# Kernel tuning notes

Measured on AMD Instinct MI355X. Metric: run time of the kernel, lower is better.

Reference implementation:

```python
import jax, jax.numpy as jnp
import numpy as np
import math

# ---- GPT-OSS attention config (gpt-oss-20b) ----
HIDDEN = 2880
HEAD_DIM = 64
N_Q_HEADS = 64
N_KV_HEADS = 8
GROUP = N_Q_HEADS // N_KV_HEADS  # 8
WINDOW = 128                      # sliding window (keys in (q-128, q])
ROPE_BASE = 150000.0
SCALING_FACTOR = 32.0
NTK_ALPHA = 1.0
NTK_BETA = 32.0
INIT_CTX = 4096
Q_SIZE = N_Q_HEADS * HEAD_DIM     # 4096
KV_SIZE = N_KV_HEADS * HEAD_DIM   # 512
SM_SCALE = HEAD_DIM ** -0.5


def _yarn_inv_freq_and_concentration():
    """YaRN-scaled inverse frequencies (matches GptOssRotaryEmbedding)."""
    d_half = HEAD_DIM / 2
    freq = ROPE_BASE ** (np.arange(0, HEAD_DIM, 2, dtype=np.float32) / HEAD_DIM)
    concentration = 0.1 * math.log(SCALING_FACTOR) + 1.0
    low = d_half * math.log(INIT_CTX / (NTK_BETA * 2 * math.pi)) / math.log(ROPE_BASE)
    high = d_half * math.log(INIT_CTX / (NTK_ALPHA * 2 * math.pi)) / math.log(ROPE_BASE)
    interpolation = 1.0 / (SCALING_FACTOR * freq)
    extrapolation = 1.0 / freq
    ramp = (np.arange(d_half, dtype=np.float32) - low) / (high - low)
    mask = 1.0 - np.clip(ramp, 0.0, 1.0)
    inv_freq = interpolation * (1.0 - mask) + extrapolation * mask
    return jnp.asarray(inv_freq, jnp.float32), jnp.float32(concentration)

_INV_FREQ, _CONC = _yarn_inv_freq_and_concentration()


def _apply_rope(x, cos, sin):
    # x: [n, h, d]; cos/sin: [n, d/2] (neox style: rotate halves)
    d2 = HEAD_DIM // 2
    x1, x2 = x[..., :d2], x[..., d2:]
    c, s = cos[:, None, :], sin[:, None, :]
    return jnp.concatenate([x1 * c - x2 * s, x2 * c + x1 * s], axis=-1)


def setup_inputs() -> dict:
    key = jax.random.key(0)
    ks = jax.random.split(key, 6)
    n = 8192
    return {
        "hidden_states": jax.random.normal(ks[0], (n, HIDDEN), jnp.float32),
        "position_ids": jnp.arange(n, dtype=jnp.int32),
        "qkv_w": jax.random.normal(ks[1], (Q_SIZE + 2 * KV_SIZE, HIDDEN), jnp.float32) * (HIDDEN ** -0.5),
        "qkv_b": jax.random.normal(ks[2], (Q_SIZE + 2 * KV_SIZE,), jnp.float32) * 0.02,
        "o_w": jax.random.normal(ks[3], (HIDDEN, Q_SIZE), jnp.float32) * (Q_SIZE ** -0.5),
        "o_b": jax.random.normal(ks[4], (HIDDEN,), jnp.float32) * 0.02,
        "sinks": jax.random.normal(ks[5], (N_Q_HEADS,), jnp.float32),
    }


def reference(hidden_states, position_ids, qkv_w, qkv_b, o_w, o_b, sinks):
    n = hidden_states.shape[0]
    W = WINDOW
    nb = n // W  # n must be a multiple of the window (8192 / 128 = 64)

    # QKV projection
    qkv = hidden_states @ qkv_w.T + qkv_b
    q = qkv[:, :Q_SIZE].reshape(n, N_Q_HEADS, HEAD_DIM)
    k = qkv[:, Q_SIZE:Q_SIZE + KV_SIZE].reshape(n, N_KV_HEADS, HEAD_DIM)
    v = qkv[:, Q_SIZE + KV_SIZE:].reshape(n, N_KV_HEADS, HEAD_DIM)

    # RoPE (YaRN, neox)
    angles = position_ids.astype(jnp.float32)[:, None] * _INV_FREQ[None, :]
    cos = jnp.cos(angles) * _CONC
    sin = jnp.sin(angles) * _CONC
    q = _apply_rope(q, cos, sin)
    k = _apply_rope(k, cos, sin)

    # Blocked sliding-window attention: each W-block of queries attends to
    # [previous block, own block] keys (window=W keys incl. self).
    qb = (q * SM_SCALE).reshape(nb, W, N_KV_HEADS, GROUP, HEAD_DIM)
    kb = k.reshape(nb, W, N_KV_HEADS, HEAD_DIM)
    vb = v.reshape(nb, W, N_KV_HEADS, HEAD_DIM)
    k2 = jnp.concatenate([jnp.concatenate([jnp.zeros_like(kb[:1]), kb[:-1]], 0), kb], axis=1)  # [nb,2W,Hk,d]
    v2 = jnp.concatenate([jnp.concatenate([jnp.zeros_like(vb[:1]), vb[:-1]], 0), vb], axis=1)

    # scores: [nb, Hk, G, W, 2W]
    scores = jnp.einsum('bqgjd,bkgd->bgjqk', qb, k2)

    # mask: key global idx = (b-1)*W + j; need 0 <= q-k <= W-1 and k >= 0
    i = jnp.arange(W)[:, None]
    j = jnp.arange(2 * W)[None, :]
    mrel = (j >= i + 1) & (j <= i + W)                       # [W, 2W]
    first = (jnp.arange(nb)[:, None, None] > 0) | (j >= W)   # [nb, 1|W, 2W]
    mask = (mrel[None] & first)[:, None, None, :, :]          # [nb,1,1,W,2W]

    neg_inf = jnp.float32(-jnp.inf)
    s = jnp.where(mask, scores, neg_inf)
    sink = sinks.reshape(N_KV_HEADS, GROUP)[None, :, :, None]  # [1,Hk,G,1]
    m = jnp.maximum(jnp.max(s, axis=-1), sink)                  # [nb,Hk,G,W]
    e = jnp.exp(s - m[..., None])
    denom = e.sum(axis=-1) + jnp.exp(sink - m)                  # sink adds to denominator only
    p = e / denom[..., None]

    out = jnp.einsum('bgjqk,bkgd->bqgjd', p, v2).reshape(n, Q_SIZE)
    return out @ o_w.T + o_b
```

## Files before the change

### kernel.cpp

```cpp
#include <hip/hip_runtime.h>
#include <math.h>
#include <stdint.h>

typedef float  f32x4  __attribute__((ext_vector_type(4)));
typedef __bf16 bf16x8 __attribute__((ext_vector_type(8)));
typedef __bf16 bf16x4 __attribute__((ext_vector_type(4)));

#define MFMA16(a, b, c) __builtin_amdgcn_mfma_f32_16x16x32_bf16(a, b, c, 0, 0, 0)

__device__ __forceinline__ void async16(const void* g, void* l) {
  __builtin_amdgcn_global_load_lds((__attribute__((address_space(1))) void*)g,
                                   (__attribute__((address_space(3))) void*)l,
                                   16, 0, 0);
}

__global__ __launch_bounds__(256) void cast_f32_to_bf16(const float* __restrict__ in,
                                                        __bf16* __restrict__ out, int n) {
  int idx = (blockIdx.x * 256 + threadIdx.x) * 4;
  if (idx + 3 < n) {
    float4 v = *(const float4*)(in + idx);
    bf16x4 o;
    o[0] = (__bf16)v.x; o[1] = (__bf16)v.y; o[2] = (__bf16)v.z; o[3] = (__bf16)v.w;
    *(bf16x4*)(out + idx) = o;
  }
}

__global__ __launch_bounds__(256) void rope_table_kernel(const int* __restrict__ pos_ids,
                                                         float2* __restrict__ tab, int total) {
  int idx = blockIdx.x * 256 + threadIdx.x;
  if (idx >= total) return;
  int p = idx >> 5, d = idx & 31;
  float posf = (float)pos_ids[p];
  float ex = (float)(2 * d) * (1.0f / 64.0f);
  float freq = powf(150000.0f, ex);
  float inv_scaled = 1.0f / (32.0f * freq);
  float inv_plain = 1.0f / freq;
  float lr = logf(150000.0f);
  const float TWO_PI = 6.28318530717958647692f;
  float low  = 32.0f * logf(4096.0f / (32.0f * TWO_PI)) / lr;
  float high = 32.0f * logf(4096.0f / TWO_PI) / lr;
  float ramp = ((float)d - low) / (high - low);
  ramp = fminf(fmaxf(ramp, 0.0f), 1.0f);
  float maskv = 1.0f - ramp;
  float inv_freq = inv_scaled * (1.0f - maskv) + inv_plain * maskv;
  float conc = 0.1f * logf(32.0f) + 1.0f;
  float ang = posf * inv_freq;
  float s, c;
  sincosf(ang, &s, &c);
  tab[idx] = make_float2(c * conc, s * conc);
}

template <typename OutT, bool DO_ROPE>
__global__ __launch_bounds__(512, 2) void gemm256(const __bf16* __restrict__ A,
                                                  const __bf16* __restrict__ B,
                                                  const float* __restrict__ bias,
                                                  OutT* __restrict__ C,
                                                  const float2* __restrict__ tab,
                                                  int M, int N, int K) {
  __shared__ __align__(16) __bf16 lds_all[65536];
  __bf16* Asl = lds_all;
  __bf16* Bsl = lds_all + 32768;

  const int tid = threadIdx.x;
  const int wv  = tid >> 6;
  const int ln  = tid & 63;
  const int l16 = ln & 15;
  const int quad = ln >> 4;
  const int wr = wv >> 2;
  const int wc = wv & 3;

  const int nTN = (N + 255) >> 8;
  int bid = (int)blockIdx.x;
  int nwg = (int)gridDim.x;
  int swz = bid;
  if ((nwg & 7) == 0) {
    int cpx = nwg >> 3;
    swz = (bid & 7) * cpx + (bid >> 3);
  }
  const int brow = swz / nTN;
  const int bcol = swz % nTN;
  const int row0 = brow << 8, col0 = bcol << 8;

  const int rsw  = (l16 >> 1) & 3;
  const int aoff = (wr * 128 + l16) * 32 + ((quad ^ rsw) * 8);
  const int boff = (wc * 64 + l16) * 32 + ((quad ^ rsw) * 8);

  const int srow = tid >> 2;
  const int skq  = (tid & 3) ^ ((tid >> 3) & 3);

  auto stA = [&](int t_, int kh) {
    const __bf16* s = A + (size_t)(row0 + srow) * K + t_ * 64 + kh * 32 + skq * 8;
    char* d = (char*)Asl + (((2 * t_ + kh) & 3) << 14) + (wv << 10);
    async16(s, d);
    async16(s + (size_t)128 * K, d + 8192);
  };
  auto stB = [&](int t_, int kh) {
    int r0 = col0 + srow;       if (r0 > N - 1) r0 = N - 1;
    int r1 = col0 + srow + 128; if (r1 > N - 1) r1 = N - 1;
    const int kb = t_ * 64 + kh * 32 + skq * 8;
    char* d = (char*)Bsl + (((2 * t_ + kh) & 3) << 14) + (wv << 10);
    async16(B + (size_t)r0 * K + kb, d);
    async16(B + (size_t)r1 * K + kb, d + 8192);
  };

  f32x4 acc[8][4];
#pragma unroll
  for (int t = 0; t < 8; t++)
#pragma unroll
    for (int u = 0; u < 4; u++) acc[t][u] = (f32x4){0.f, 0.f, 0.f, 0.f};

  const int nt = K >> 6;

  stA(0, 0); stB(0, 0); stA(0, 1); stB(0, 1);
  if (nt > 1) {
    stA(1, 0); stB(1, 0); stA(1, 1); stB(1, 1);
    asm volatile("s_waitcnt vmcnt(4)" ::: "memory");
  } else {
    asm volatile("s_waitcnt vmcnt(0)" ::: "memory");
  }
  __builtin_amdgcn_s_barrier();

#define PHASE_TAIL()                                      \
  __builtin_amdgcn_s_barrier();                           \
  asm volatile("s_waitcnt lgkmcnt(0)" ::: "memory");      \
  __builtin_amdgcn_sched_barrier(0);                      \
  __builtin_amdgcn_s_setprio(1);

#define PHASE_END()                                       \
  __builtin_amdgcn_s_setprio(0);                          \
  __builtin_amdgcn_s_barrier();

#pragma unroll 1
  for (int t = 0; t < nt; ++t) {
    const __bf16* As0 = Asl + (((2 * t) & 3) << 13);
    const __bf16* Bs0 = Bsl + (((2 * t) & 3) << 13);
    const __bf16* As1 = Asl + (((2 * t + 1) & 3) << 13);
    const __bf16* Bs1 = Bsl + (((2 * t + 1) & 3) << 13);
    bf16x8 a[8], b0, b1;

#pragma unroll
    for (int tt = 0; tt < 8; ++tt) a[tt] = *(const bf16x8*)(As0 + aoff + tt * 512);
    b0 = *(const bf16x8*)(Bs0 + boff);
    b1 = *(const bf16x8*)(Bs0 + boff + 512);
    if (t >= 1 && t + 1 < nt) stA(t + 1, 1);
    PHASE_TAIL();
#pragma unroll
    for (int tt = 0; tt < 8; ++tt) {
      acc[tt][0] = MFMA16(a[tt], b0, acc[tt][0]);
      acc[tt][1] = MFMA16(a[tt], b1, acc[tt][1]);
    }
    PHASE_END();

    b0 = *(const bf16x8*)(Bs0 + boff + 1024);
    b1 = *(const bf16x8*)(Bs0 + boff + 1536);
    if (t >= 1 && t + 1 < nt) stB(t + 1, 1);
    PHASE_TAIL();
#pragma unroll
    for (int tt = 0; tt < 8; ++tt) {
      acc[tt][2] = MFMA16(a[tt], b0, acc[tt][2]);
      acc[tt][3] = MFMA16(a[tt], b1, acc[tt][3]);
    }
    PHASE_END();

#pragma unroll
    for (int tt = 0; tt < 8; ++tt) a[tt] = *(const bf16x8*)(As1 + aoff + tt * 512);
    b0 = *(const bf16x8*)(Bs1 + boff);
    b1 = *(const bf16x8*)(Bs1 + boff + 512);
    if (t + 2 < nt) stA(t + 2, 0);
    PHASE_TAIL();
#pragma unroll
    for (int tt = 0; tt < 8; ++tt) {
      acc[tt][0] = MFMA16(a[tt], b0, acc[tt][0]);
      acc[tt][1] = MFMA16(a[tt], b1, acc[tt][1]);
    }
    PHASE_END();

    b0 = *(const bf16x8*)(Bs1 + boff + 1024);
    b1 = *(const bf16x8*)(Bs1 + boff + 1536);
    if (t + 2 < nt) {
      stB(t + 2, 0);
      asm volatile("s_waitcnt vmcnt(4)" ::: "memory");
    } else {
      asm volatile("s_waitcnt vmcnt(0)" ::: "memory");
    }
    PHASE_TAIL();
#pragma unroll
    for (int tt = 0; tt < 8; ++tt) {
      acc[tt][2] = MFMA16(a[tt], b0, acc[tt][2]);
      acc[tt][3] = MFMA16(a[tt], b1, acc[tt][3]);
    }
    PHASE_END();
  }
#undef PHASE_TAIL
#undef PHASE_END

  const int hh = (col0 + wc * 64) >> 6;
  if (DO_ROPE && hh < 72) {
    const float scale = hh < 64 ? 0.125f : 1.0f;
    float bv[4];
#pragma unroll
    for (int u = 0; u < 4; u++) bv[u] = bias[col0 + wc * 64 + u * 16 + l16];
#pragma unroll
    for (int tt = 0; tt < 8; ++tt) {
      int rowb = row0 + wr * 128 + tt * 16 + quad * 4;
#pragma unroll
      for (int r = 0; r < 4; r++) {
        int row = rowb + r;
#pragma unroll
        for (int u = 0; u < 2; u++) {
          float2 cs = tab[row * 32 + u * 16 + l16];
          float x1 = acc[tt][u][r] + bv[u];
          float x2 = acc[tt][u + 2][r] + bv[u + 2];
          C[(size_t)row * N + col0 + wc * 64 + u * 16 + l16] =
              (OutT)((x1 * cs.x - x2 * cs.y) * scale);
          C[(size_t)row * N + col0 + wc * 64 + (u + 2) * 16 + l16] =
              (OutT)((x2 * cs.x + x1 * cs.y) * scale);
        }
      }
    }
  } else {
#pragma unroll
    for (int u = 0; u < 4; u++) {
      int col = col0 + wc * 64 + u * 16 + l16;
      if (col < N) {
        float bv = bias[col];
#pragma unroll
        for (int tt = 0; tt < 8; ++tt) {
          int row = row0 + wr * 128 + tt * 16 + quad * 4;
#pragma unroll
          for (int r = 0; r < 4; r++)
            C[(size_t)(row + r) * N + col] = (OutT)(acc[tt][u][r] + bv);
        }
      }
    }
  }
}

__global__ __launch_bounds__(256) void attn_kernel(const __bf16* __restrict__ qkv,
                                                   const float* __restrict__ sinks,
                                                   __bf16* __restrict__ out) {
  __shared__ __align__(16) __bf16 vT_s[64 * 264];
  __shared__ __align__(16) __bf16 p_s[64 * 136];
  const int tid = threadIdx.x;
  const int bh = blockIdx.x >> 1;
  const int qh = blockIdx.x & 1;
  const int b = bh >> 3;
  const int h = bh & 7;
  const int wv = tid >> 6;
  const int ln = tid & 63;
  const int l16 = ln & 15;
  const int quad = ln >> 4;

  for (int c = tid; c < 2048; c += 256) {
    int key = c >> 3, dc = c & 7;
    int vpos = b * 128 + key - 128;
    bf16x8 vv = {};
    if (vpos >= 0)
      vv = *(const bf16x8*)(qkv + (size_t)vpos * 5120 + 4608 + h * 64 + dc * 8);
    int keysw = key ^ ((dc & 3) << 3);
#pragma unroll
    for (int l2 = 0; l2 < 8; l2++)
      vT_s[(dc * 8 + l2) * 264 + keysw] = vv[l2];
  }
  __syncthreads();

#pragma unroll 1
  for (int pass = 0; pass < 8; pass++) {
    int g = qh * 4 + (pass >> 1);
    int i0 = (pass & 1) * 64 + wv * 16;
    int head = h * 8 + g;
    float sink = sinks[head];

    size_t qbase = (size_t)(b * 128 + i0 + l16) * 5120 + head * 64;
    bf16x8 aq0 = *(const bf16x8*)(qkv + qbase + quad * 8);
    bf16x8 aq1 = *(const bf16x8*)(qkv + qbase + 32 + quad * 8);

    f32x4 sc[16];
#pragma unroll
    for (int ct = 0; ct < 16; ct++) {
      int key = ct * 16 + l16;
      int kpos = b * 128 + key - 128;
      if (kpos < 0) kpos = 0;
      const __bf16* kp = qkv + (size_t)kpos * 5120 + 4096 + h * 64;
      bf16x8 kb0 = *(const bf16x8*)(kp + quad * 8);
      bf16x8 kb1 = *(const bf16x8*)(kp + 32 + quad * 8);
      f32x4 z = (f32x4){0.f, 0.f, 0.f, 0.f};
      __builtin_amdgcn_s_setprio(1);
      z = MFMA16(aq0, kb0, z);
      z = MFMA16(aq1, kb1, z);
      __builtin_amdgcn_s_setprio(0);
      sc[ct] = z;
    }

    float mx[4] = {-INFINITY, -INFINITY, -INFINITY, -INFINITY};
#pragma unroll
    for (int ct = 0; ct < 16; ct++) {
      int j = ct * 16 + l16;
#pragma unroll
      for (int r = 0; r < 4; r++) {
        int i = i0 + quad * 4 + r;
        bool valid = (j >= i + 1) && (j <= i + 128) && (b > 0 || j >= 128);
        float s = valid ? sc[ct][r] : -INFINITY;
        sc[ct][r] = s;
        mx[r] = fmaxf(mx[r], s);
      }
    }
#pragma unroll
    for (int off = 1; off < 16; off <<= 1)
#pragma unroll
      for (int r = 0; r < 4; r++)
        mx[r] = fmaxf(mx[r], __shfl_xor(mx[r], off));
#pragma unroll
    for (int r = 0; r < 4; r++) mx[r] = fmaxf(mx[r], sink);

    float sum[4] = {0.f, 0.f, 0.f, 0.f};
#pragma unroll
    for (int ct = 0; ct < 16; ct++)
#pragma unroll
      for (int r = 0; r < 4; r++) {
        float e = __expf(sc[ct][r] - mx[r]);
        sc[ct][r] = e;
        sum[r] += e;
      }
#pragma unroll
    for (int off = 1; off < 16; off <<= 1)
#pragma unroll
      for (int r = 0; r < 4; r++)
        sum[r] += __shfl_xor(sum[r], off);

    f32x4 o[4];
#pragma unroll
    for (int dt = 0; dt < 4; dt++) o[dt] = (f32x4){0.f, 0.f, 0.f, 0.f};
#pragma unroll 1
    for (int kh = 0; kh < 2; kh++) {
#pragma unroll
      for (int ct = 0; ct < 8; ct++)
#pragma unroll
        for (int r = 0; r < 4; r++)
          p_s[(wv * 16 + quad * 4 + r) * 136 + ct * 16 + l16] = (__bf16)sc[kh * 8 + ct][r];
#pragma unroll
      for (int ks = 0; ks < 4; ks++) {
        bf16x8 pa = *(const bf16x8*)&p_s[(wv * 16 + l16) * 136 + ks * 32 + quad * 8];
        __builtin_amdgcn_s_setprio(1);
#pragma unroll
        for (int dt = 0; dt < 4; dt++) {
          int sw = ((dt * 2 + (l16 >> 3)) & 3) << 3;
          bf16x8 vb = *(const bf16x8*)&vT_s[(dt * 16 + l16) * 264 +
                                            ((kh * 128 + ks * 32 + quad * 8) ^ sw)];
          o[dt] = MFMA16(pa, vb, o[dt]);
        }
        __builtin_amdgcn_s_setprio(0);
      }
    }

#pragma unroll
    for (int r = 0; r < 4; r++) {
      float rd = 1.0f / (sum[r] + __expf(sink - mx[r]));
      int posn = b * 128 + i0 + quad * 4 + r;
      size_t obase = (size_t)posn * 4096 + head * 64;
#pragma unroll
      for (int dt = 0; dt < 4; dt++)
        out[obase + dt * 16 + l16] = (__bf16)(o[dt][r] * rd);
    }
  }
}

extern "C" void kernel_launch(void* const* d_in, const int* in_sizes, int n_in,
                              void* d_out, int out_size, void* d_ws, size_t ws_size,
                              hipStream_t stream) {
  (void)in_sizes; (void)n_in; (void)out_size; (void)ws_size;
  const float* hs     = (const float*)d_in[0];
  const int*   pos    = (const int*)d_in[1];
  const float* qkv_w  = (const float*)d_in[2];
  const float* qkv_b  = (const float*)d_in[3];
  const float* o_w    = (const float*)d_in[4];
  const float* o_b    = (const float*)d_in[5];
  const float* sinks  = (const float*)d_in[6];
  float* outp = (float*)d_out;
  char* ws = (char*)d_ws;

  const size_t O_QKV = 0;
  const size_t O_ATT = 83886080;
  const size_t O_TAB = 131072000;
  const size_t O_W   = 150994944;
  __bf16* qkvb = (__bf16*)(ws + O_QKV);
  __bf16* hsb  = (__bf16*)(ws + O_ATT);
  __bf16* attn = (__bf16*)(ws + O_ATT);
  float2* tab  = (float2*)(ws + O_TAB);
  __bf16* wb   = (__bf16*)(ws + O_W);

  cast_f32_to_bf16<<<23040, 256, 0, stream>>>(hs, hsb, 8192 * 2880);
  cast_f32_to_bf16<<<14400, 256, 0, stream>>>(qkv_w, wb, 5120 * 2880);
  rope_table_kernel<<<1024, 256, 0, stream>>>(pos, tab, 8192 * 32);
  gemm256<__bf16, true><<<640, 512, 0, stream>>>(hsb, wb, qkv_b, qkvb, tab,
                                                 8192, 5120, 2880);
  cast_f32_to_bf16<<<11520, 256, 0, stream>>>(o_w, wb, 2880 * 4096);
  attn_kernel<<<1024, 256, 0, stream>>>(qkvb, sinks, attn);
  gemm256<float, false><<<384, 512, 0, stream>>>(attn, wb, o_b, outp, nullptr,
                                                 8192, 2880, 4096);
}
```

Baseline: 926.4 us.

## Stage K in swizzled LDS for attention and reorder GEMM MFMA phases

The attention kernel now loads the K window into a swizzled shared-memory tile once per block, alongside V, instead of reading K from global memory in every pass. This removes repeated global loads of the same keys across the eight passes. The P staging buffer is shrunk by processing keys in four chunks of 64 rather than two of 128. The GEMM main loop is reorganised into 4x4 MFMA quadrants that reload A fragments instead of B fragments, and the sched_barrier is dropped so the compiler can interleave LDS reads with MFMAs, at the cost of more LDS use and different register pressure.

```diff
diff --git a/kernel.cpp b/kernel.cpp
--- a/kernel.cpp
+++ b/kernel.cpp
@@ -123,7 +123,6 @@
 #define PHASE_TAIL()                                      \
   __builtin_amdgcn_s_barrier();                           \
   asm volatile("s_waitcnt lgkmcnt(0)" ::: "memory");      \
-  __builtin_amdgcn_sched_barrier(0);                      \
   __builtin_amdgcn_s_setprio(1);
 
 #define PHASE_END()                                       \
@@ -136,47 +135,44 @@
     const __bf16* Bs0 = Bsl + (((2 * t) & 3) << 13);
     const __bf16* As1 = Asl + (((2 * t + 1) & 3) << 13);
     const __bf16* Bs1 = Bsl + (((2 * t + 1) & 3) << 13);
-    bf16x8 a[8], b0, b1;
-
-#pragma unroll
-    for (int tt = 0; tt < 8; ++tt) a[tt] = *(const bf16x8*)(As0 + aoff + tt * 512);
-    b0 = *(const bf16x8*)(Bs0 + boff);
-    b1 = *(const bf16x8*)(Bs0 + boff + 512);
+    bf16x8 a[4], b[4];
+
+#pragma unroll
+    for (int i = 0; i < 4; ++i) a[i] = *(const bf16x8*)(As0 + aoff + i * 512);
+#pragma unroll
+    for (int u = 0; u < 4; ++u) b[u] = *(const bf16x8*)(Bs0 + boff + u * 512);
     if (t >= 1 && t + 1 < nt) stA(t + 1, 1);
     PHASE_TAIL();
 #pragma unroll
-    for (int tt = 0; tt < 8; ++tt) {
-      acc[tt][0] = MFMA16(a[tt], b0, acc[tt][0]);
-      acc[tt][1] = MFMA16(a[tt], b1, acc[tt][1]);
-    }
+    for (int i = 0; i < 4; ++i)
+#pragma unroll
+      for (int u = 0; u < 4; ++u) acc[i][u] = MFMA16(a[i], b[u], acc[i][u]);
     PHASE_END();
 
-    b0 = *(const bf16x8*)(Bs0 + boff + 1024);
-    b1 = *(const bf16x8*)(Bs0 + boff + 1536);
+#pragma unroll
+    for (int i = 0; i < 4; ++i) a[i] = *(const bf16x8*)(As0 + aoff + (4 + i) * 512);
     if (t >= 1 && t + 1 < nt) stB(t + 1, 1);
     PHASE_TAIL();
 #pragma unroll
-    for (int tt = 0; tt < 8; ++tt) {
-      acc[tt][2] = MFMA16(a[tt], b0, acc[tt][2]);
-      acc[tt][3] = MFMA16(a[tt], b1, acc[tt][3]);
-    }
+    for (int i = 0; i < 4; ++i)
+#pragma unroll
+      for (int u = 0; u < 4; ++u) acc[4 + i][u] = MFMA16(a[i], b[u], acc[4 + i][u]);
     PHASE_END();
 
 #pragma unroll
-    for (int tt = 0; tt < 8; ++tt) a[tt] = *(const bf16x8*)(As1 + aoff + tt * 512);
-    b0 = *(const bf16x8*)(Bs1 + boff);
-    b1 = *(const bf16x8*)(Bs1 + boff + 512);
+    for (int i = 0; i < 4; ++i) a[i] = *(const bf16x8*)(As1 + aoff + i * 512);
+#pragma unroll
+    for (int u = 0; u < 4; ++u) b[u] = *(const bf16x8*)(Bs1 + boff + u * 512);
     if (t + 2 < nt) stA(t + 2, 0);
     PHASE_TAIL();
 #pragma unroll
-    for (int tt = 0; tt < 8; ++tt) {
-      acc[tt][0] = MFMA16(a[tt], b0, acc[tt][0]);
-      acc[tt][1] = MFMA16(a[tt], b1, acc[tt][1]);
-    }
+    for (int i = 0; i < 4; ++i)
+#pragma unroll
+      for (int u = 0; u < 4; ++u) acc[i][u] = MFMA16(a[i], b[u], acc[i][u]);
     PHASE_END();
 
-    b0 = *(const bf16x8*)(Bs1 + boff + 1024);
-    b1 = *(const bf16x8*)(Bs1 + boff + 1536);
+#pragma unroll
+    for (int i = 0; i < 4; ++i) a[i] = *(const bf16x8*)(As1 + aoff + (4 + i) * 512);
     if (t + 2 < nt) {
       stB(t + 2, 0);
       asm volatile("s_waitcnt vmcnt(4)" ::: "memory");
@@ -185,10 +181,9 @@
     }
     PHASE_TAIL();
 #pragma unroll
-    for (int tt = 0; tt < 8; ++tt) {
-      acc[tt][2] = MFMA16(a[tt], b0, acc[tt][2]);
-      acc[tt][3] = MFMA16(a[tt], b1, acc[tt][3]);
-    }
+    for (int i = 0; i < 4; ++i)
+#pragma unroll
+      for (int u = 0; u < 4; ++u) acc[4 + i][u] = MFMA16(a[i], b[u], acc[4 + i][u]);
     PHASE_END();
   }
 #undef PHASE_TAIL
@@ -240,7 +235,8 @@
                                                    const float* __restrict__ sinks,
                                                    __bf16* __restrict__ out) {
   __shared__ __align__(16) __bf16 vT_s[64 * 264];
-  __shared__ __align__(16) __bf16 p_s[64 * 136];
+  __shared__ __align__(16) __bf16 k_s[256 * 64];
+  __shared__ __align__(16) __bf16 p_s[64 * 72];
   const int tid = threadIdx.x;
   const int bh = blockIdx.x >> 1;
   const int qh = blockIdx.x & 1;
@@ -253,14 +249,18 @@
 
   for (int c = tid; c < 2048; c += 256) {
     int key = c >> 3, dc = c & 7;
-    int vpos = b * 128 + key - 128;
-    bf16x8 vv = {};
-    if (vpos >= 0)
-      vv = *(const bf16x8*)(qkv + (size_t)vpos * 5120 + 4608 + h * 64 + dc * 8);
+    int pos = b * 128 + key - 128;
+    bf16x8 vv = {}, kk = {};
+    if (pos >= 0) {
+      const __bf16* base = qkv + (size_t)pos * 5120 + h * 64 + dc * 8;
+      kk = *(const bf16x8*)(base + 4096);
+      vv = *(const bf16x8*)(base + 4608);
+    }
     int keysw = key ^ ((dc & 3) << 3);
 #pragma unroll
     for (int l2 = 0; l2 < 8; l2++)
       vT_s[(dc * 8 + l2) * 264 + keysw] = vv[l2];
+    *(bf16x8*)&k_s[key * 64 + ((dc ^ (key & 7)) * 8)] = kk;
   }
   __syncthreads();
 
@@ -276,14 +276,12 @@
     bf16x8 aq1 = *(const bf16x8*)(qkv + qbase + 32 + quad * 8);
 
     f32x4 sc[16];
+    const int sw0 = (quad ^ (l16 & 7)) * 8;
 #pragma unroll
     for (int ct = 0; ct < 16; ct++) {
-      int key = ct * 16 + l16;
-      int kpos = b * 128 + key - 128;
-      if (kpos < 0) kpos = 0;
-      const __bf16* kp = qkv + (size_t)kpos * 5120 + 4096 + h * 64;
-      bf16x8 kb0 = *(const bf16x8*)(kp + quad * 8);
-      bf16x8 kb1 = *(const bf16x8*)(kp + 32 + quad * 8);
+      const __bf16* kp = &k_s[(ct * 16 + l16) * 64];
+      bf16x8 kb0 = *(const bf16x8*)(kp + sw0);
+      bf16x8 kb1 = *(const bf16x8*)(kp + (sw0 ^ 32));
       f32x4 z = (f32x4){0.f, 0.f, 0.f, 0.f};
       __builtin_amdgcn_s_setprio(1);
       z = MFMA16(aq0, kb0, z);
@@ -331,22 +329,22 @@
     f32x4 o[4];
 #pragma unroll
     for (int dt = 0; dt < 4; dt++) o[dt] = (f32x4){0.f, 0.f, 0.f, 0.f};
-#pragma unroll 1
-    for (int kh = 0; kh < 2; kh++) {
-#pragma unroll
-      for (int ct = 0; ct < 8; ct++)
+#pragma unroll
+    for (int q = 0; q < 4; q++) {
+#pragma unroll
+      for (int ct = 0; ct < 4; ct++)
 #pragma unroll
         for (int r = 0; r < 4; r++)
-          p_s[(wv * 16 + quad * 4 + r) * 136 + ct * 16 + l16] = (__bf16)sc[kh * 8 + ct][r];
-#pragma unroll
-      for (int ks = 0; ks < 4; ks++) {
-        bf16x8 pa = *(const bf16x8*)&p_s[(wv * 16 + l16) * 136 + ks * 32 + quad * 8];
+          p_s[(wv * 16 + quad * 4 + r) * 72 + ct * 16 + l16] = (__bf16)sc[q * 4 + ct][r];
+#pragma unroll
+      for (int ks = 0; ks < 2; ks++) {
+        bf16x8 pa = *(const bf16x8*)&p_s[(wv * 16 + l16) * 72 + ks * 32 + quad * 8];
         __builtin_amdgcn_s_setprio(1);
 #pragma unroll
         for (int dt = 0; dt < 4; dt++) {
+          int kk = q * 64 + ks * 32 + quad * 8;
           int sw = ((dt * 2 + (l16 >> 3)) & 3) << 3;
-          bf16x8 vb = *(const bf16x8*)&vT_s[(dt * 16 + l16) * 264 +
-                                            ((kh * 128 + ks * 32 + quad * 8) ^ sw)];
+          bf16x8 vb = *(const bf16x8*)&vT_s[(dt * 16 + l16) * 264 + (kk ^ sw)];
           o[dt] = MFMA16(pa, vb, o[dt]);
         }
         __builtin_amdgcn_s_setprio(0);
```

New measurement: 814.1 us. -12.1%, faster.
